# Kernel tuning notes

Measured on AMD Instinct MI355X. Metric: run time of the kernel, lower is better.

## Reference

```python
import jax, jax.numpy as jnp
import numpy as np

DIM = 512
NUM_HEADS = 8
HEAD_DIM = DIM // NUM_HEADS          # 64
KEY_DIM = int(HEAD_DIM * 0.5)        # 32
H_QKV = DIM + NUM_HEADS * KEY_DIM * 2  # 1024
SCALE = KEY_DIM ** -0.5
EPS = 1e-5


def bn(x, gamma, beta, mean, var):
    # inference-mode BatchNorm2d over channel axis 1 of NCHW
    inv = gamma / jnp.sqrt(var + EPS)
    return x * inv[None, :, None, None] + (beta - mean * inv)[None, :, None, None]


def conv1x1(x, w):
    # w: [out, in] (1x1 conv collapsed); x: NCHW
    return jnp.einsum('bchw,oc->bohw', x, w)


def dwconv3x3(x, w):
    # depthwise 3x3, 'same' padding; w: [C,1,3,3]
    return jax.lax.conv_general_dilated(
        x, w, window_strides=(1, 1), padding='SAME',
        feature_group_count=x.shape[1],
        dimension_numbers=('NCHW', 'OIHW', 'NCHW'))


def setup_inputs() -> dict:
    key = jax.random.key(0)
    ks = jax.random.split(key, 16)
    B, C, H, W = 8, DIM, 40, 40
    f = jax.random.normal
    inp = {
        'x': f(ks[0], (B, C, H, W), jnp.float32),
        'qkv_w': f(ks[1], (H_QKV, DIM), jnp.float32) * (1.0 / np.sqrt(DIM)),
        'qkv_gamma': 1.0 + 0.1 * f(ks[2], (H_QKV,), jnp.float32),
        'qkv_beta': 0.1 * f(ks[3], (H_QKV,), jnp.float32),
        'qkv_mean': 0.1 * f(ks[4], (H_QKV,), jnp.float32),
        'qkv_var': jax.random.uniform(ks[5], (H_QKV,), jnp.float32) + 0.5,
        'pe_w': f(ks[6], (DIM, 1, 3, 3), jnp.float32) * (1.0 / 3.0),
        'pe_gamma': 1.0 + 0.1 * f(ks[7], (DIM,), jnp.float32),
        'pe_beta': 0.1 * f(ks[8], (DIM,), jnp.float32),
        'pe_mean': 0.1 * f(ks[9], (DIM,), jnp.float32),
        'pe_var': jax.random.uniform(ks[10], (DIM,), jnp.float32) + 0.5,
        'proj_w': f(ks[11], (DIM, DIM), jnp.float32) * (1.0 / np.sqrt(DIM)),
        'proj_gamma': 1.0 + 0.1 * f(ks[12], (DIM,), jnp.float32),
        'proj_beta': 0.1 * f(ks[13], (DIM,), jnp.float32),
        'proj_mean': 0.1 * f(ks[14], (DIM,), jnp.float32),
        'proj_var': jax.random.uniform(ks[15], (DIM,), jnp.float32) + 0.5,
    }
    return inp


def reference(x, qkv_w, qkv_gamma, qkv_beta, qkv_mean, qkv_var,
              pe_w, pe_gamma, pe_beta, pe_mean, pe_var,
              proj_w, proj_gamma, proj_beta, proj_mean, proj_var):
    B, C, H, W = x.shape
    N = H * W
    qkv = bn(conv1x1(x, qkv_w), qkv_gamma, qkv_beta, qkv_mean, qkv_var)
    qkv = qkv.reshape(B, NUM_HEADS, KEY_DIM * 2 + HEAD_DIM, N)
    q = qkv[:, :, :KEY_DIM]                    # [B,h,kd,N]
    k = qkv[:, :, KEY_DIM:2 * KEY_DIM]         # [B,h,kd,N]
    v = qkv[:, :, 2 * KEY_DIM:]                # [B,h,hd,N]
    # attn = q^T @ k * scale -> [B,h,N,N], softmax over last dim
    attn = jnp.einsum('bhkn,bhkm->bhnm', q, k) * SCALE
    attn = jax.nn.softmax(attn, axis=-1)
    # out = v @ attn^T -> [B,h,hd,N]
    out = jnp.einsum('bhdm,bhnm->bhdn', v, attn).reshape(B, C, H, W)
    pe = bn(dwconv3x3(v.reshape(B, C, H, W), pe_w), pe_gamma, pe_beta, pe_mean, pe_var)
    y = out + pe
    y = bn(conv1x1(y, proj_w), proj_gamma, proj_beta, proj_mean, proj_var)
    return y
```

## Files before the change

### kernel.cpp

```cpp
#include <hip/hip_runtime.h>
#include <hip/hip_bf16.h>

#define EPS 1e-5f
#define SCALE 0.17677669529663687f
#define QSCALE 0.25500526817095634f

typedef __attribute__((ext_vector_type(8))) short bf16x8;
typedef __attribute__((ext_vector_type(4))) float f32x4;
typedef __attribute__((ext_vector_type(8))) unsigned short u16x8;

__device__ __forceinline__ unsigned short f2bf(float x) {
  union { float f; unsigned int u; } a; a.f = x;
  unsigned int r = a.u + 0x7FFFu + ((a.u >> 16) & 1u);
  return (unsigned short)(r >> 16);
}
__device__ __forceinline__ float bf2f(unsigned short u) {
  union { unsigned int u; float f; } a; a.u = ((unsigned int)u) << 16;
  return a.f;
}

__device__ __forceinline__ float fexp2(float x) {
#if __has_builtin(__builtin_amdgcn_exp2f)
  return __builtin_amdgcn_exp2f(x);
#else
  float r; asm("v_exp_f32 %0, %1" : "=v"(r) : "v"(x)); return r;
#endif
}

__device__ __forceinline__ void gload_lds16(const void* g, void* l) {
  __builtin_amdgcn_global_load_lds(
      (const __attribute__((address_space(1))) unsigned int*)g,
      (__attribute__((address_space(3))) unsigned int*)l, 16, 0, 0);
}

__device__ __forceinline__ unsigned int pack_bf_trunc(float a, float b) {
  return __builtin_amdgcn_perm(__float_as_uint(b), __float_as_uint(a), 0x07060302u);
}

__global__ __launch_bounds__(256) void cast_w_kernel(
    const float* __restrict__ qw, const float* __restrict__ pw,
    short* __restrict__ wq, short* __restrict__ wp) {
  int idx = blockIdx.x * 256 + threadIdx.x;
  const float4* src;
  ushort4* dst;
  if (idx < 131072) {
    src = (const float4*)qw + idx;
    dst = (ushort4*)wq + idx;
  } else {
    src = (const float4*)pw + (idx - 131072);
    dst = (ushort4*)wp + (idx - 131072);
  }
  float4 v = *src;
  ushort4 u;
  u.x = f2bf(v.x); u.y = f2bf(v.y); u.z = f2bf(v.z); u.w = f2bf(v.w);
  *dst = u;
}

__global__ __launch_bounds__(256) void transpose_cast_kernel(
    const float* __restrict__ X, short* __restrict__ XT) {
  __shared__ unsigned short T[64][72];
  const int b = blockIdx.z, c0 = blockIdx.x * 64, n0 = blockIdx.y * 64;
  const int t = threadIdx.x, nl = t & 63, w = t >> 6;
#pragma unroll
  for (int ci = 0; ci < 16; ++ci) {
    int cl = ci * 4 + w;
    T[nl][cl] = f2bf(X[((size_t)(b * 512 + c0 + cl)) * 1600 + n0 + nl]);
  }
  __syncthreads();
  const int n2 = t >> 2, cg = (t & 3) * 16;
  unsigned short* o = (unsigned short*)XT + ((size_t)(b * 1600 + n0 + n2)) * 512 + c0 + cg;
  *(u16x8*)&o[0] = *(const u16x8*)&T[n2][cg];
  *(u16x8*)&o[8] = *(const u16x8*)&T[n2][cg + 8];
}

__global__ __launch_bounds__(256) void transpose16_kernel(
    const short* __restrict__ S, short* __restrict__ D) {
  __shared__ unsigned short T[64][72];
  const int b = blockIdx.z, c0 = blockIdx.x * 64, n0 = blockIdx.y * 64;
  const int t = threadIdx.x, nl = t & 63, w = t >> 6;
  const unsigned short* Sp = (const unsigned short*)S;
#pragma unroll
  for (int ci = 0; ci < 16; ++ci) {
    int cl = ci * 4 + w;
    T[nl][cl] = Sp[((size_t)(b * 512 + c0 + cl)) * 1600 + n0 + nl];
  }
  __syncthreads();
  const int n2 = t >> 2, cg = (t & 3) * 16;
  unsigned short* o = (unsigned short*)D + ((size_t)(b * 1600 + n0 + n2)) * 512 + c0 + cg;
  *(u16x8*)&o[0] = *(const u16x8*)&T[n2][cg];
  *(u16x8*)&o[8] = *(const u16x8*)&T[n2][cg + 8];
}

__global__ __launch_bounds__(256) void qkv_mfma_kernel(
    const short* __restrict__ XT, const short* __restrict__ WQ,
    const float* __restrict__ gamma, const float* __restrict__ beta,
    const float* __restrict__ mean, const float* __restrict__ var,
    short* __restrict__ qT, short* __restrict__ kT, short* __restrict__ vb) {
  __shared__ __align__(16) unsigned short As[128 * 32];
  __shared__ __align__(16) unsigned short Bs[128 * 32];

  const int t = threadIdx.x, w = t >> 6, lane = t & 63;
  const int quad = lane >> 4, l16 = lane & 15;
  const int wr = w >> 1, wc = w & 1;
  const int ngt = blockIdx.x, h = blockIdx.y;
  const int o0 = h * 128, ng0 = ngt * 128;

  const int srow = lane >> 2;
  const int sseg = (lane & 3) * 8;

  f32x4 acc[4][4];
#pragma unroll
  for (int mi = 0; mi < 4; ++mi)
#pragma unroll
    for (int nj = 0; nj < 4; ++nj) { acc[mi][nj][0]=0.f; acc[mi][nj][1]=0.f; acc[mi][nj][2]=0.f; acc[mi][nj][3]=0.f; }

  for (int kt = 0; kt < 16; ++kt) {
    const int c0 = kt * 32;
    if (kt) __syncthreads();
#pragma unroll
    for (int r = 0; r < 2; ++r) {
      const int row = (r * 4 + w) * 16 + srow;
      gload_lds16(WQ + (size_t)(o0 + row) * 512 + c0 + sseg, As + (r * 4 + w) * 512);
      gload_lds16(XT + (size_t)(ng0 + row) * 512 + c0 + sseg, Bs + (r * 4 + w) * 512);
    }
    __syncthreads();
    bf16x8 af[4], bfr[4];
#pragma unroll
    for (int i = 0; i < 4; ++i) {
      af[i]  = *(const bf16x8*)&As[(wr * 64 + i * 16 + l16) * 32 + quad * 8];
      bfr[i] = *(const bf16x8*)&Bs[(wc * 64 + i * 16 + l16) * 32 + quad * 8];
    }
#pragma unroll
    for (int mi = 0; mi < 4; ++mi)
#pragma unroll
      for (int nj = 0; nj < 4; ++nj)
        acc[mi][nj] = __builtin_amdgcn_mfma_f32_16x16x32_bf16(af[mi], bfr[nj], acc[mi][nj], 0, 0, 0);
  }

  const int ng_base = ng0 + wc * 64;
#pragma unroll
  for (int mi = 0; mi < 4; ++mi) {
    const int ol = wr * 64 + mi * 16 + quad * 4;
    const int ob = o0 + ol;
    float inv[4], add[4];
#pragma unroll
    for (int r = 0; r < 4; ++r) {
      inv[r] = gamma[ob + r] * rsqrtf(var[ob + r] + EPS);
      add[r] = beta[ob + r] - mean[ob + r] * inv[r];
    }
    const int region = wr * 2 + (mi >> 1);
    if (region == 0) {
      const int kk = mi * 16 + quad * 4;
#pragma unroll
      for (int nj = 0; nj < 4; ++nj) {
        int ng = ng_base + nj * 16 + l16;
        int b = ng / 1600, n = ng - b * 1600;
        ushort4 u;
        u.x = f2bf((acc[mi][nj][0] * inv[0] + add[0]) * QSCALE);
        u.y = f2bf((acc[mi][nj][1] * inv[1] + add[1]) * QSCALE);
        u.z = f2bf((acc[mi][nj][2] * inv[2] + add[2]) * QSCALE);
        u.w = f2bf((acc[mi][nj][3] * inv[3] + add[3]) * QSCALE);
        *(ushort4*)&qT[((size_t)(b * 8 + h) * 1600 + n) * 32 + kk] = u;
      }
    } else if (region == 1) {
      const int kk = (mi - 2) * 16 + quad * 4;
#pragma unroll
      for (int nj = 0; nj < 4; ++nj) {
        int ng = ng_base + nj * 16 + l16;
        int b = ng / 1600, n = ng - b * 1600;
        ushort4 u;
        u.x = f2bf(acc[mi][nj][0] * inv[0] + add[0]);
        u.y = f2bf(acc[mi][nj][1] * inv[1] + add[1]);
        u.z = f2bf(acc[mi][nj][2] * inv[2] + add[2]);
        u.w = f2bf(acc[mi][nj][3] * inv[3] + add[3]);
        *(ushort4*)&kT[((size_t)(b * 8 + h) * 1600 + n) * 32 + kk] = u;
      }
    } else {
      const int ch = h * 64 + (ol - 64);
#pragma unroll
      for (int nj = 0; nj < 4; ++nj) {
        int ng = ng_base + nj * 16 + l16;
        int b = ng / 1600, n = ng - b * 1600;
#pragma unroll
        for (int r = 0; r < 4; ++r)
          ((unsigned short*)vb)[((size_t)(b * 512 + ch + r)) * 1600 + n] =
              f2bf(acc[mi][nj][r] * inv[r] + add[r]);
      }
    }
  }
}

__global__ __launch_bounds__(256) void attn_mfma_kernel(
    const short* __restrict__ qT, const short* __restrict__ kT,
    const short* __restrict__ vb, short* __restrict__ ybf) {
  const int N = 1600;
  const int PS = 72;
  __shared__ __align__(16) unsigned short Plds[2][64 * PS];
  __shared__ float den_lds[4][64];
  __shared__ float rden[64];

  const int t = threadIdx.x;
  const int w = t >> 6, lane = t & 63, quad = lane >> 4, l16 = lane & 15;
  const int bh = blockIdx.x, b = bh >> 3, h = bh & 7;
  const int n0 = blockIdx.y * 64;

  const short* qTb = qT + (size_t)(b * 8 + h) * N * 32;
  const short* kTb = kT + (size_t)(b * 8 + h) * N * 32;
  const short* vbb = vb + ((size_t)b * 512 + h * 64 + w * 16) * N;

  bf16x8 qf[4];
#pragma unroll
  for (int i = 0; i < 4; ++i)
    qf[i] = *(const bf16x8*)(qTb + (size_t)(n0 + i * 16 + l16) * 32 + quad * 8);

  f32x4 acc[4];
#pragma unroll
  for (int i = 0; i < 4; ++i) { acc[i][0]=0.f; acc[i][1]=0.f; acc[i][2]=0.f; acc[i][3]=0.f; }
  float den[4] = {0.f, 0.f, 0.f, 0.f};
  const f32x4 zero4 = {0.f, 0.f, 0.f, 0.f};

#pragma unroll 2
  for (int mt = 0; mt < 25; ++mt) {
    const int m0 = mt * 64;
    unsigned short* Pb = &Plds[mt & 1][0];
    bf16x8 kf = *(const bf16x8*)(kTb + (size_t)(m0 + w * 16 + l16) * 32 + quad * 8);
#pragma unroll
    for (int i = 0; i < 4; ++i) {
      f32x4 s = __builtin_amdgcn_mfma_f32_16x16x32_bf16(kf, qf[i], zero4, 0, 0, 0);
      float p0 = fexp2(s[0]), p1 = fexp2(s[1]), p2 = fexp2(s[2]), p3 = fexp2(s[3]);
      den[i] += (p0 + p1) + (p2 + p3);
      uint2 pk;
      pk.x = pack_bf_trunc(p0, p1);
      pk.y = pack_bf_trunc(p2, p3);
      *(uint2*)&Pb[(size_t)(i * 16 + l16) * PS + w * 16 + quad * 4] = pk;
    }
    __syncthreads();
#pragma unroll
    for (int c = 0; c < 2; ++c) {
      bf16x8 vfr = *(const bf16x8*)(vbb + (size_t)l16 * N + m0 + c * 32 + quad * 8);
#pragma unroll
      for (int i = 0; i < 4; ++i) {
        bf16x8 pf = *(const bf16x8*)(Pb + (size_t)(i * 16 + l16) * PS + c * 32 + quad * 8);
        acc[i] = __builtin_amdgcn_mfma_f32_16x16x32_bf16(pf, vfr, acc[i], 0, 0, 0);
      }
    }
  }

#pragma unroll
  for (int i = 0; i < 4; ++i) {
    den[i] += __shfl_xor(den[i], 16, 64);
    den[i] += __shfl_xor(den[i], 32, 64);
  }
  if (quad == 0) {
#pragma unroll
    for (int i = 0; i < 4; ++i)
      den_lds[w][i * 16 + l16] = den[i];
  }
  __syncthreads();
  if (t < 64)
    rden[t] = 1.f / (den_lds[0][t] + den_lds[1][t] + den_lds[2][t] + den_lds[3][t]);
  __syncthreads();

  unsigned short* yr = (unsigned short*)ybf +
      ((size_t)b * 512 + h * 64 + w * 16 + l16) * N + n0;
#pragma unroll
  for (int i = 0; i < 4; ++i) {
    const int nb = i * 16 + quad * 4;
    ushort4 o4;
    o4.x = f2bf(acc[i][0] * rden[nb + 0]);
    o4.y = f2bf(acc[i][1] * rden[nb + 1]);
    o4.z = f2bf(acc[i][2] * rden[nb + 2]);
    o4.w = f2bf(acc[i][3] * rden[nb + 3]);
    *(ushort4*)&yr[nb] = o4;
  }
}

__global__ __launch_bounds__(256) void pe_kernel(
    const short* __restrict__ Ybf, const short* __restrict__ VB,
    const float* __restrict__ pw,
    const float* __restrict__ gamma, const float* __restrict__ beta,
    const float* __restrict__ mean, const float* __restrict__ var,
    short* __restrict__ YB) {
  __shared__ __align__(16) unsigned short V[4 * 42 * 56];
  __shared__ float wlds[36];
  __shared__ float invs[4], adds[4];

  const int t = threadIdx.x;
  const int b = blockIdx.y, c0 = blockIdx.x * 4;

  const u16x8 z = {0, 0, 0, 0, 0, 0, 0, 0};
  for (int k = t; k < 1176; k += 256)
    *(u16x8*)&V[k * 8] = z;
  if (t < 36) wlds[t] = pw[c0 * 9 + t];
  if (t < 4) {
    int c = c0 + t;
    float inv = gamma[c] * rsqrtf(var[c] + EPS);
    invs[t] = inv;
    adds[t] = beta[c] - mean[c] * inv;
  }
  __syncthreads();

  for (int u = t; u < 800; u += 256) {
    int ch = u / 200, j = u - ch * 200;
    int row = j / 5, col8 = (j - row * 5) * 8;
    u16x8 d = *(const u16x8*)((const unsigned short*)VB +
        ((size_t)(b * 512 + c0 + ch) * 1600 + row * 40 + col8));
    *(u16x8*)&V[ch * 2352 + (row + 1) * 56 + 8 + col8] = d;
  }
  __syncthreads();

#pragma unroll 1
  for (int k = 0; k < 25; ++k) {
    int o = k * 256 + t;
    int ch = o / 1600, n = o - ch * 1600;
    int hh = n / 40, ww = n - hh * 40;
    const unsigned short* Vc = &V[ch * 2352 + (hh + 1) * 56 + 8 + ww];
    const float* wk = &wlds[ch * 9];
    float s = 0.f;
#pragma unroll
    for (int dy = 0; dy < 3; ++dy)
#pragma unroll
      for (int dx = 0; dx < 3; ++dx)
        s += wk[dy * 3 + dx] * bf2f(Vc[(dy - 1) * 56 + (dx - 1)]);
    size_t idx = (size_t)(b * 512 + c0 + ch) * 1600 + n;
    float val = bf2f(((const unsigned short*)Ybf)[idx]) + s * invs[ch] + adds[ch];
    YB[idx] = (short)f2bf(val);
  }
}

__global__ __launch_bounds__(256) void proj_mfma_kernel(
    const short* __restrict__ YT, const short* __restrict__ WP,
    const float* __restrict__ gamma, const float* __restrict__ beta,
    const float* __restrict__ mean, const float* __restrict__ var,
    float* __restrict__ OUT) {
  __shared__ __align__(16) unsigned short As[64 * 32];
  __shared__ __align__(16) unsigned short Bs[128 * 32];

  const int t = threadIdx.x, w = t >> 6, lane = t & 63;
  const int quad = lane >> 4, l16 = lane & 15;
  const int wr = w >> 1, wc = w & 1;
  const int ngt = blockIdx.x;
  const int o0 = blockIdx.y * 64;
  const int ng0 = ngt * 128;

  const int srow = lane >> 2;
  const int sseg = (lane & 3) * 8;

  f32x4 acc[2][4];
#pragma unroll
  for (int mi = 0; mi < 2; ++mi)
#pragma unroll
    for (int nj = 0; nj < 4; ++nj) { acc[mi][nj][0]=0.f; acc[mi][nj][1]=0.f; acc[mi][nj][2]=0.f; acc[mi][nj][3]=0.f; }

  for (int kt = 0; kt < 16; ++kt) {
    const int c0 = kt * 32;
    if (kt) __syncthreads();
    {
      const int row = w * 16 + srow;
      gload_lds16(WP + (size_t)(o0 + row) * 512 + c0 + sseg, As + w * 512);
    }
#pragma unroll
    for (int r = 0; r < 2; ++r) {
      const int row = (r * 4 + w) * 16 + srow;
      gload_lds16(YT + (size_t)(ng0 + row) * 512 + c0 + sseg, Bs + (r * 4 + w) * 512);
    }
    __syncthreads();
    bf16x8 af[2], bfr[4];
#pragma unroll
    for (int i = 0; i < 2; ++i)
      af[i] = *(const bf16x8*)&As[(wr * 32 + i * 16 + l16) * 32 + quad * 8];
#pragma unroll
    for (int i = 0; i < 4; ++i)
      bfr[i] = *(const bf16x8*)&Bs[(wc * 64 + i * 16 + l16) * 32 + quad * 8];
#pragma unroll
    for (int mi = 0; mi < 2; ++mi)
#pragma unroll
      for (int nj = 0; nj < 4; ++nj)
        acc[mi][nj] = __builtin_amdgcn_mfma_f32_16x16x32_bf16(af[mi], bfr[nj], acc[mi][nj], 0, 0, 0);
  }

  const int ng_base = ng0 + wc * 64;
#pragma unroll
  for (int mi = 0; mi < 2; ++mi) {
    const int ob = o0 + wr * 32 + mi * 16 + quad * 4;
    float inv[4], add[4];
#pragma unroll
    for (int r = 0; r < 4; ++r) {
      inv[r] = gamma[ob + r] * rsqrtf(var[ob + r] + EPS);
      add[r] = beta[ob + r] - mean[ob + r] * inv[r];
    }
#pragma unroll
    for (int nj = 0; nj < 4; ++nj) {
      int ng = ng_base + nj * 16 + l16;
      int b = ng / 1600, n = ng - b * 1600;
#pragma unroll
      for (int r = 0; r < 4; ++r)
        OUT[((size_t)(b * 512 + ob + r)) * 1600 + n] = acc[mi][nj][r] * inv[r] + add[r];
    }
  }
}

extern "C" void kernel_launch(void* const* d_in, const int* in_sizes, int n_in,
                              void* d_out, int out_size, void* d_ws, size_t ws_size,
                              hipStream_t stream) {
  const float* x          = (const float*)d_in[0];
  const float* qkv_w      = (const float*)d_in[1];
  const float* qkv_gamma  = (const float*)d_in[2];
  const float* qkv_beta   = (const float*)d_in[3];
  const float* qkv_mean   = (const float*)d_in[4];
  const float* qkv_var    = (const float*)d_in[5];
  const float* pe_w       = (const float*)d_in[6];
  const float* pe_gamma   = (const float*)d_in[7];
  const float* pe_beta    = (const float*)d_in[8];
  const float* pe_mean    = (const float*)d_in[9];
  const float* pe_var     = (const float*)d_in[10];
  const float* proj_w     = (const float*)d_in[11];
  const float* proj_gamma = (const float*)d_in[12];
  const float* proj_beta  = (const float*)d_in[13];
  const float* proj_mean  = (const float*)d_in[14];
  const float* proj_var   = (const float*)d_in[15];
  float* out = (float*)d_out;

  float* ws_a = (float*)d_ws;
  short* ybf_attn = (short*)d_ws;
  short* qT   = (short*)(ws_a + (size_t)6553600);
  short* kT   = qT + (size_t)3276800;
  short* vb   = kT + (size_t)3276800;
  short* xT   = vb + (size_t)6553600;
  short* wq   = xT + (size_t)6553600;
  short* wp   = wq + (size_t)524288;
  short* yT   = xT;
  short* ybf_pe = qT;

  cast_w_kernel<<<768, 256, 0, stream>>>(qkv_w, proj_w, wq, wp);
  {
    dim3 grid(8, 25, 8), block(256);
    transpose_cast_kernel<<<grid, block, 0, stream>>>(x, xT);
  }
  {
    dim3 grid(100, 8), block(256);
    qkv_mfma_kernel<<<grid, block, 0, stream>>>(
        xT, wq, qkv_gamma, qkv_beta, qkv_mean, qkv_var, qT, kT, vb);
  }
  {
    dim3 grid(64, 25), block(256);
    attn_mfma_kernel<<<grid, block, 0, stream>>>(qT, kT, vb, ybf_attn);
  }
  {
    dim3 grid(128, 8), block(256);
    pe_kernel<<<grid, block, 0, stream>>>(
        ybf_attn, vb, pe_w, pe_gamma, pe_beta, pe_mean, pe_var, ybf_pe);
  }
  {
    dim3 grid(8, 25, 8), block(256);
    transpose16_kernel<<<grid, block, 0, stream>>>(ybf_pe, yT);
  }
  {
    dim3 grid(100, 8), block(256);
    proj_mfma_kernel<<<grid, block, 0, stream>>>(
        yT, wp, proj_gamma, proj_beta, proj_mean, proj_var, out);
  }
}
```

Baseline: 237.8 us.

## Keep attention P in registers per wave, dropping LDS staging and block barriers

```diff
diff --git a/kernel.cpp b/kernel.cpp
--- a/kernel.cpp
+++ b/kernel.cpp
@@ -194,84 +194,69 @@
     const short* __restrict__ qT, const short* __restrict__ kT,
     const short* __restrict__ vb, short* __restrict__ ybf) {
   const int N = 1600;
-  const int PS = 72;
-  __shared__ __align__(16) unsigned short Plds[2][64 * PS];
-  __shared__ float den_lds[4][64];
-  __shared__ float rden[64];
-
   const int t = threadIdx.x;
   const int w = t >> 6, lane = t & 63, quad = lane >> 4, l16 = lane & 15;
   const int bh = blockIdx.x, b = bh >> 3, h = bh & 7;
-  const int n0 = blockIdx.y * 64;
-
-  const short* qTb = qT + (size_t)(b * 8 + h) * N * 32;
-  const short* kTb = kT + (size_t)(b * 8 + h) * N * 32;
-  const short* vbb = vb + ((size_t)b * 512 + h * 64 + w * 16) * N;
-
-  bf16x8 qf[4];
-#pragma unroll
-  for (int i = 0; i < 4; ++i)
-    qf[i] = *(const bf16x8*)(qTb + (size_t)(n0 + i * 16 + l16) * 32 + quad * 8);
+  const int n0w = blockIdx.y * 64 + w * 16;
+
+  const unsigned short* qTb = (const unsigned short*)qT + (size_t)bh * N * 32;
+  const unsigned short* kTb = (const unsigned short*)kT + (size_t)bh * N * 32;
+  const unsigned short* vbb = (const unsigned short*)vb + ((size_t)b * 512 + h * 64) * N;
+
+  const bf16x8 qf = *(const bf16x8*)(qTb + (size_t)(n0w + l16) * 32 + quad * 8);
 
   f32x4 acc[4];
 #pragma unroll
   for (int i = 0; i < 4; ++i) { acc[i][0]=0.f; acc[i][1]=0.f; acc[i][2]=0.f; acc[i][3]=0.f; }
-  float den[4] = {0.f, 0.f, 0.f, 0.f};
+  float den = 0.f;
   const f32x4 zero4 = {0.f, 0.f, 0.f, 0.f};
 
+  const unsigned short* krow = kTb + (size_t)l16 * 32 + quad * 8;
+
 #pragma unroll 2
-  for (int mt = 0; mt < 25; ++mt) {
-    const int m0 = mt * 64;
-    unsigned short* Pb = &Plds[mt & 1][0];
-    bf16x8 kf = *(const bf16x8*)(kTb + (size_t)(m0 + w * 16 + l16) * 32 + quad * 8);
+  for (int mt = 0; mt < 50; ++mt) {
+    const int m0 = mt * 32;
+    const bf16x8 kf0 = *(const bf16x8*)(krow + (size_t)m0 * 32);
+    const bf16x8 kf1 = *(const bf16x8*)(krow + (size_t)(m0 + 16) * 32);
+    f32x4 s0 = __builtin_amdgcn_mfma_f32_16x16x32_bf16(kf0, qf, zero4, 0, 0, 0);
+    f32x4 s1 = __builtin_amdgcn_mfma_f32_16x16x32_bf16(kf1, qf, zero4, 0, 0, 0);
+    float p0 = fexp2(s0[0]), p1 = fexp2(s0[1]), p2 = fexp2(s0[2]), p3 = fexp2(s0[3]);
+    float p4 = fexp2(s1[0]), p5 = fexp2(s1[1]), p6 = fexp2(s1[2]), p7 = fexp2(s1[3]);
+    den += ((p0 + p1) + (p2 + p3)) + ((p4 + p5) + (p6 + p7));
+
+    union { bf16x8 v; uint4 u; } pk;
+    pk.u.x = pack_bf_trunc(p0, p1);
+    pk.u.y = pack_bf_trunc(p2, p3);
+    pk.u.z = pack_bf_trunc(p4, p5);
+    pk.u.w = pack_bf_trunc(p6, p7);
+
 #pragma unroll
     for (int i = 0; i < 4; ++i) {
-      f32x4 s = __builtin_amdgcn_mfma_f32_16x16x32_bf16(kf, qf[i], zero4, 0, 0, 0);
-      float p0 = fexp2(s[0]), p1 = fexp2(s[1]), p2 = fexp2(s[2]), p3 = fexp2(s[3]);
-      den[i] += (p0 + p1) + (p2 + p3);
-      uint2 pk;
-      pk.x = pack_bf_trunc(p0, p1);
-      pk.y = pack_bf_trunc(p2, p3);
-      *(uint2*)&Pb[(size_t)(i * 16 + l16) * PS + w * 16 + quad * 4] = pk;
-    }
-    __syncthreads();
-#pragma unroll
-    for (int c = 0; c < 2; ++c) {
-      bf16x8 vfr = *(const bf16x8*)(vbb + (size_t)l16 * N + m0 + c * 32 + quad * 8);
-#pragma unroll
-      for (int i = 0; i < 4; ++i) {
-        bf16x8 pf = *(const bf16x8*)(Pb + (size_t)(i * 16 + l16) * PS + c * 32 + quad * 8);
-        acc[i] = __builtin_amdgcn_mfma_f32_16x16x32_bf16(pf, vfr, acc[i], 0, 0, 0);
-      }
-    }
-  }
-
+      const unsigned short* vr = vbb + (size_t)(i * 16 + l16) * N + m0 + 4 * quad;
+      uint2 lo = *(const uint2*)vr;
+      uint2 hi = *(const uint2*)(vr + 16);
+      union { bf16x8 v; uint4 u; } vv;
+      vv.u.x = lo.x; vv.u.y = lo.y; vv.u.z = hi.x; vv.u.w = hi.y;
+      acc[i] = __builtin_amdgcn_mfma_f32_16x16x32_bf16(pk.v, vv.v, acc[i], 0, 0, 0);
+    }
+  }
+
+  den += __shfl_xor(den, 16, 64);
+  den += __shfl_xor(den, 32, 64);
+  const float rden = 1.f / den;
+  float dv[4];
+#pragma unroll
+  for (int r = 0; r < 4; ++r) dv[r] = __shfl(rden, quad * 4 + r, 64);
+
+  unsigned short* yb = (unsigned short*)ybf + ((size_t)b * 512 + h * 64) * N;
 #pragma unroll
   for (int i = 0; i < 4; ++i) {
-    den[i] += __shfl_xor(den[i], 16, 64);
-    den[i] += __shfl_xor(den[i], 32, 64);
-  }
-  if (quad == 0) {
-#pragma unroll
-    for (int i = 0; i < 4; ++i)
-      den_lds[w][i * 16 + l16] = den[i];
-  }
-  __syncthreads();
-  if (t < 64)
-    rden[t] = 1.f / (den_lds[0][t] + den_lds[1][t] + den_lds[2][t] + den_lds[3][t]);
-  __syncthreads();
-
-  unsigned short* yr = (unsigned short*)ybf +
-      ((size_t)b * 512 + h * 64 + w * 16 + l16) * N + n0;
-#pragma unroll
-  for (int i = 0; i < 4; ++i) {
-    const int nb = i * 16 + quad * 4;
     ushort4 o4;
-    o4.x = f2bf(acc[i][0] * rden[nb + 0]);
-    o4.y = f2bf(acc[i][1] * rden[nb + 1]);
-    o4.z = f2bf(acc[i][2] * rden[nb + 2]);
-    o4.w = f2bf(acc[i][3] * rden[nb + 3]);
-    *(ushort4*)&yr[nb] = o4;
+    o4.x = f2bf(acc[i][0] * dv[0]);
+    o4.y = f2bf(acc[i][1] * dv[1]);
+    o4.z = f2bf(acc[i][2] * dv[2]);
+    o4.w = f2bf(acc[i][3] * dv[3]);
+    *(ushort4*)&yb[(size_t)(i * 16 + l16) * N + n0w + quad * 4] = o4;
   }
 }
 
```

Measured after the change: 521.4 us. 2.19x slower.
